# Optimization experiments

Measured on AMD Instinct MI355X. Metric: run time of the kernel, lower is better.

The kernel has to match this reference:

```python
import jax, jax.numpy as jnp
import numpy as np

# HP constants (mirroring the torch module's HP)
NUM_EFFECTIVE_QUEUES = 2
DISCOUNT_FACTOR = 0.995
USE_MIN_FOR_LOSS_REDUCE = False
ENTROPY_COEF = 0.0  # entropy branch disabled, matching HP.ENTROPY_COEF = 0.0

N_CLAUSES = 50000
FEAT_DIM = 64
HIDDEN = 256
KEY_DIM = 256
T_SEL = 1000  # number of SEL events in the journal
NEG_INF = -1e30


def setup_inputs() -> dict:
    key = jax.random.key(0)
    ks = jax.random.split(key, 10)
    feature_vecs = jax.random.normal(ks[0], (N_CLAUSES, FEAT_DIM), dtype=jnp.float32)
    W1 = jax.random.normal(ks[1], (FEAT_DIM, HIDDEN), dtype=jnp.float32) / np.sqrt(FEAT_DIM)
    b1 = jnp.zeros((HIDDEN,), dtype=jnp.float32)
    W2 = jax.random.normal(ks[2], (HIDDEN, KEY_DIM), dtype=jnp.float32) / np.sqrt(HIDDEN)
    b2 = jnp.zeros((KEY_DIM,), dtype=jnp.float32)
    keys_W = jax.random.normal(ks[3], (NUM_EFFECTIVE_QUEUES, KEY_DIM), dtype=jnp.float32) / np.sqrt(KEY_DIM)
    # Per-SEL-event passive set (equivalent to replaying ADD/REM events host-side):
    passive_mask = jax.random.uniform(ks[4], (T_SEL, N_CLAUSES)) < 0.10
    # proof_flas membership per clause, good = passive & proof
    proof = jax.random.uniform(ks[5], (N_CLAUSES,)) < 0.05
    good_mask = passive_mask & proof[None, :]
    # queue index = time % NUM_EFFECTIVE_QUEUES, time increments per SEL event
    queue_idx = jnp.arange(T_SEL, dtype=jnp.int32) % NUM_EFFECTIVE_QUEUES
    return {
        "feature_vecs": feature_vecs, "W1": W1, "b1": b1, "W2": W2, "b2": b2,
        "keys_W": keys_W, "passive_mask": passive_mask, "good_mask": good_mask,
        "queue_idx": queue_idx,
    }


def reference(feature_vecs, W1, b1, W2, b2, keys_W, passive_mask, good_mask, queue_idx):
    # clause_embedder: 2-layer MLP
    h = jax.nn.relu(feature_vecs @ W1 + b1)         # [N, H]
    emb = h @ W2 + b2                                # [N, K]
    logits = keys_W @ emb.T                          # [Q, N]
    ev_logits = logits[queue_idx]                    # [T, N] gather per SEL event

    num_good = good_mask.sum(axis=-1)                # [T]
    num_pass = passive_mask.sum(axis=-1)             # [T]
    num_bad = num_pass - num_good
    valid = (num_good > 0) & (num_bad > 0)           # events contributing loss

    # log_softmax restricted to the passive set
    masked = jnp.where(passive_mask, ev_logits, NEG_INF)
    lsm = jax.nn.log_softmax(masked, axis=-1)        # [T, N]

    # cross_entropy = -mean(lsm over good idxs)  (USE_MIN_FOR_LOSS_REDUCE = False)
    good_sum = jnp.where(good_mask, lsm, 0.0).sum(axis=-1)
    ce = -good_sum / jnp.maximum(num_good, 1).astype(lsm.dtype)

    # factor *= DISCOUNT_FACTOR after each counted step
    steps_before = (jnp.cumsum(valid.astype(jnp.int32)) - valid.astype(jnp.int32))
    factor = jnp.asarray(DISCOUNT_FACTOR, lsm.dtype) ** steps_before.astype(lsm.dtype)

    weight = factor * (num_bad.astype(lsm.dtype) / jnp.maximum(num_pass, 1).astype(lsm.dtype))
    loss_terms = jnp.where(valid, weight * ce, 0.0)
    steps = valid.sum().astype(lsm.dtype)
    loss = loss_terms.sum() / jnp.maximum(steps, 1.0)
    return loss.reshape(1)
```

## Files before the change

kernel.cpp:

```cpp
#include <hip/hip_runtime.h>
#include <hip/hip_bf16.h>

#define N_CL   50000
#define FEAT   64
#define HID    256
#define KD     256
#define T_SEL  1000
#define JSPLIT 4
#define JPB    (HID / JSPLIT)
#define NBLK   782
#define DCHUNK 10

#define WK_OFF  0
#define CK_OFF  512
#define MQ_OFF  514
#define P_OFF   520
#define LG_OFF  (P_OFF + JSPLIT * 2 * N_CL)
#define ACC_OFF (LG_OFF + 2 * N_CL)

__device__ __forceinline__ unsigned fkey(float f) {
    unsigned u = __float_as_uint(f);
    return (u & 0x80000000u) ? ~u : (u | 0x80000000u);
}
__device__ __forceinline__ float finv(unsigned k) {
    unsigned u = (k & 0x80000000u) ? (k ^ 0x80000000u) : ~k;
    return __uint_as_float(u);
}

__global__ __launch_bounds__(256) void prep_kernel(
        const float* __restrict__ W2, const float* __restrict__ b2,
        const float* __restrict__ keysW,
        float* __restrict__ wk, float* __restrict__ ck,
        unsigned* __restrict__ mq, float* __restrict__ acc) {
    __shared__ float sk0[KD], sk1[KD], sb2[KD], red[256];
    int tid = threadIdx.x;
    sk0[tid] = keysW[tid];
    sk1[tid] = keysW[KD + tid];
    sb2[tid] = b2[tid];
    for (int i = tid; i < T_SEL * 4; i += 256) acc[i] = 0.0f;
    if (tid < 2) mq[tid] = 0u;
    __syncthreads();

    const float* w2r = W2 + (size_t)tid * KD;
    float a0 = 0.f, a1 = 0.f;
    #pragma unroll 4
    for (int k = 0; k < KD; k++) {
        float w = w2r[k];
        a0 = fmaf(w, sk0[k], a0);
        a1 = fmaf(w, sk1[k], a1);
    }
    wk[tid * 2 + 0] = a0;
    wk[tid * 2 + 1] = a1;

    red[tid] = sk0[tid] * sb2[tid];
    __syncthreads();
    for (int s = 128; s > 0; s >>= 1) { if (tid < s) red[tid] += red[tid + s]; __syncthreads(); }
    if (tid == 0) ck[0] = red[0];
    __syncthreads();
    red[tid] = sk1[tid] * sb2[tid];
    __syncthreads();
    for (int s = 128; s > 0; s >>= 1) { if (tid < s) red[tid] += red[tid + s]; __syncthreads(); }
    if (tid == 0) ck[1] = red[0];
}

__global__ __launch_bounds__(64) void mlp_kernel(
        const float* __restrict__ X, const float* __restrict__ W1,
        const float* __restrict__ b1, const float* __restrict__ wk,
        float* __restrict__ P) {
    int nb = blockIdx.x % NBLK;
    int p  = blockIdx.x / NBLK;
    int n  = nb * 64 + threadIdx.x;
    int nc = (n < N_CL) ? n : (N_CL - 1);

    float x[FEAT];
    const float4* xp = (const float4*)(X + (size_t)nc * FEAT);
    #pragma unroll
    for (int k4 = 0; k4 < FEAT / 4; k4++) {
        float4 v = xp[k4];
        x[4 * k4 + 0] = v.x; x[4 * k4 + 1] = v.y;
        x[4 * k4 + 2] = v.z; x[4 * k4 + 3] = v.w;
    }

    float l0 = 0.f, l1 = 0.f;
    int j0 = p * JPB;
    for (int jg = 0; jg < JPB; jg += 16) {
        float h[16];
        #pragma unroll
        for (int u = 0; u < 16; u++) h[u] = b1[j0 + jg + u];
        #pragma unroll 4
        for (int k = 0; k < FEAT; k++) {
            const float* w1r = W1 + (size_t)k * HID + j0 + jg;
            float xv = x[k];
            #pragma unroll
            for (int u = 0; u < 16; u++) h[u] = fmaf(xv, w1r[u], h[u]);
        }
        #pragma unroll
        for (int u = 0; u < 16; u++) {
            float hv = fmaxf(h[u], 0.0f);
            l0 = fmaf(hv, wk[(j0 + jg + u) * 2 + 0], l0);
            l1 = fmaf(hv, wk[(j0 + jg + u) * 2 + 1], l1);
        }
    }
    if (n < N_CL) {
        P[((size_t)p * 2 + 0) * N_CL + n] = l0;
        P[((size_t)p * 2 + 1) * N_CL + n] = l1;
    }
}

__global__ __launch_bounds__(256) void logits_fin(
        const float* __restrict__ P, const float* __restrict__ ck,
        float* __restrict__ lg, unsigned* __restrict__ mq) {
    int n = blockIdx.x * 256 + threadIdx.x;
    float m0 = -1e30f, m1 = -1e30f;
    if (n < N_CL) {
        float l0 = ck[0], l1 = ck[1];
        #pragma unroll
        for (int p = 0; p < JSPLIT; p++) {
            l0 += P[((size_t)p * 2 + 0) * N_CL + n];
            l1 += P[((size_t)p * 2 + 1) * N_CL + n];
        }
        lg[n]        = l0;
        lg[N_CL + n] = l1;
        m0 = l0; m1 = l1;
    }
    for (int off = 32; off; off >>= 1) {
        m0 = fmaxf(m0, __shfl_xor(m0, off));
        m1 = fmaxf(m1, __shfl_xor(m1, off));
    }
    __shared__ float sm0[4], sm1[4];
    int w = threadIdx.x >> 6;
    if ((threadIdx.x & 63) == 0) { sm0[w] = m0; sm1[w] = m1; }
    __syncthreads();
    if (threadIdx.x == 0) {
        m0 = fmaxf(fmaxf(sm0[0], sm0[1]), fmaxf(sm0[2], sm0[3]));
        m1 = fmaxf(fmaxf(sm1[0], sm1[1]), fmaxf(sm1[2], sm1[3]));
        atomicMax(mq + 0, fkey(m0));
        atomicMax(mq + 1, fkey(m1));
    }
}

__global__ __launch_bounds__(256) void event_kernel(
        const int* __restrict__ pass, const int* __restrict__ good,
        const int* __restrict__ qidx, const float* __restrict__ lg,
        const unsigned* __restrict__ mq, float* __restrict__ acc) {
    int t = blockIdx.x / DCHUNK;
    int c = blockIdx.x % DCHUNK;
    int q = qidx[t] & 1;
    float M = finv(mq[q]);
    const float4* lrow = (const float4*)(lg + (size_t)q * N_CL);
    const int4*   prow = (const int4*)(pass + (size_t)t * N_CL);
    const int4*   grow = (const int4*)(good + (size_t)t * N_CL);

    float s = 0.f, sg = 0.f;
    int np = 0, ng = 0;
    for (int i = c * 256 + (int)threadIdx.x; i < N_CL / 4; i += DCHUNK * 256) {
        int4   p = prow[i];
        int4   g = grow[i];
        float4 l = lrow[i];
        np += p.x + p.y + p.z + p.w;
        ng += g.x + g.y + g.z + g.w;
        float e0 = __expf(l.x - M), e1 = __expf(l.y - M);
        float e2 = __expf(l.z - M), e3 = __expf(l.w - M);
        s  = fmaf((float)p.x, e0, s);
        s  = fmaf((float)p.y, e1, s);
        s  = fmaf((float)p.z, e2, s);
        s  = fmaf((float)p.w, e3, s);
        sg = fmaf((float)g.x, l.x, sg);
        sg = fmaf((float)g.y, l.y, sg);
        sg = fmaf((float)g.z, l.z, sg);
        sg = fmaf((float)g.w, l.w, sg);
    }
    for (int off = 32; off; off >>= 1) {
        s  += __shfl_xor(s, off);
        sg += __shfl_xor(sg, off);
        np += __shfl_xor(np, off);
        ng += __shfl_xor(ng, off);
    }
    __shared__ float rs[4], rsg[4];
    __shared__ int   rnp[4], rng[4];
    int w = threadIdx.x >> 6;
    if ((threadIdx.x & 63) == 0) { rs[w] = s; rsg[w] = sg; rnp[w] = np; rng[w] = ng; }
    __syncthreads();
    if (threadIdx.x == 0) {
        s  = rs[0] + rs[1] + rs[2] + rs[3];
        sg = rsg[0] + rsg[1] + rsg[2] + rsg[3];
        np = rnp[0] + rnp[1] + rnp[2] + rnp[3];
        ng = rng[0] + rng[1] + rng[2] + rng[3];
        atomicAdd(&acc[t * 4 + 0], s);
        atomicAdd(&acc[t * 4 + 1], sg);
        atomicAdd(&acc[t * 4 + 2], (float)np);
        atomicAdd(&acc[t * 4 + 3], (float)ng);
    }
}

__global__ __launch_bounds__(1024) void final_kernel(
        const int* __restrict__ qidx, const float* __restrict__ acc,
        const unsigned* __restrict__ mq, float* __restrict__ out) {
    int t = threadIdx.x;
    float s = 0.f, sg = 0.f, np = 0.f, ng = 0.f;
    int q = 0;
    if (t < T_SEL) {
        const float* a = acc + t * 4;
        s = a[0]; sg = a[1]; np = a[2]; ng = a[3];
        q = qidx[t] & 1;
    }
    float M  = finv(mq[q]);
    float nb = np - ng;
    int valid = (t < T_SEL) && (ng > 0.5f) && (nb > 0.5f);

    __shared__ int sc[1024];
    sc[t] = valid;
    __syncthreads();
    for (int off = 1; off < 1024; off <<= 1) {
        int v = (t >= off) ? sc[t - off] : 0;
        __syncthreads();
        sc[t] += v;
        __syncthreads();
    }
    int sb    = sc[t] - valid;
    int steps = sc[1023];

    float ce   = logf(s) + M - sg / fmaxf(ng, 1.0f);
    float wgt  = powf(0.995f, (float)sb) * nb / fmaxf(np, 1.0f);
    float term = valid ? wgt * ce : 0.0f;

    __shared__ float sf[1024];
    sf[t] = term;
    __syncthreads();
    for (int off = 512; off; off >>= 1) {
        if (t < off) sf[t] += sf[t + off];
        __syncthreads();
    }
    if (t == 0) out[0] = sf[0] / fmaxf((float)steps, 1.0f);
}

extern "C" void kernel_launch(void* const* d_in, const int* in_sizes, int n_in,
                              void* d_out, int out_size, void* d_ws, size_t ws_size,
                              hipStream_t stream) {
    const float* X     = (const float*)d_in[0];
    const float* W1    = (const float*)d_in[1];
    const float* b1    = (const float*)d_in[2];
    const float* W2    = (const float*)d_in[3];
    const float* b2    = (const float*)d_in[4];
    const float* keysW = (const float*)d_in[5];
    const int*   pass  = (const int*)d_in[6];
    const int*   good  = (const int*)d_in[7];
    const int*   qidx  = (const int*)d_in[8];

    float*    ws  = (float*)d_ws;
    float*    wk  = ws + WK_OFF;
    float*    ck  = ws + CK_OFF;
    unsigned* mq  = (unsigned*)(ws + MQ_OFF);
    float*    P   = ws + P_OFF;
    float*    lg  = ws + LG_OFF;
    float*    acc = ws + ACC_OFF;
    float*    out = (float*)d_out;

    hipLaunchKernelGGL(prep_kernel, dim3(1), dim3(256), 0, stream,
                       W2, b2, keysW, wk, ck, mq, acc);
    hipLaunchKernelGGL(mlp_kernel, dim3(NBLK * JSPLIT), dim3(64), 0, stream,
                       X, W1, b1, wk, P);
    hipLaunchKernelGGL(logits_fin, dim3((N_CL + 255) / 256), dim3(256), 0, stream,
                       P, ck, lg, mq);
    hipLaunchKernelGGL(event_kernel, dim3(T_SEL * DCHUNK), dim3(256), 0, stream,
                       pass, good, qidx, lg, mq, acc);
    hipLaunchKernelGGL(final_kernel, dim3(1), dim3(1024), 0, stream,
                       qidx, acc, mq, out);
}
```

Measured before the change: 161.8 us.

## Fuse logits finalize into MLP block reduction and halve event-kernel grid

The MLP kernel now uses 256-thread blocks where each wave handles a quarter of the hidden units, then reduces partials in shared memory and writes logits and the per-queue max directly. This removes the separate logits_fin kernel and the partial-sum buffer round trip. The event kernel switches from 10 chunks per event to 2 contiguous halves with a fixed-trip unrolled loop, and writes per-block partials instead of using atomics, so final_kernel sums two slots and the accumulator zeroing is dropped. Fewer, larger blocks in the event kernel may reduce memory-level parallelism on the dominant streaming pass over the masks.

```diff
diff --git a/kernel.cpp b/kernel.cpp
--- a/kernel.cpp
+++ b/kernel.cpp
@@ -6,16 +6,14 @@
 #define HID    256
 #define KD     256
 #define T_SEL  1000
-#define JSPLIT 4
-#define JPB    (HID / JSPLIT)
 #define NBLK   782
-#define DCHUNK 10
+#define ECHUNK 6250
+#define EFULL  24
 
 #define WK_OFF  0
 #define CK_OFF  512
 #define MQ_OFF  514
-#define P_OFF   520
-#define LG_OFF  (P_OFF + JSPLIT * 2 * N_CL)
+#define LG_OFF  520
 #define ACC_OFF (LG_OFF + 2 * N_CL)
 
 __device__ __forceinline__ unsigned fkey(float f) {
@@ -31,13 +29,12 @@
         const float* __restrict__ W2, const float* __restrict__ b2,
         const float* __restrict__ keysW,
         float* __restrict__ wk, float* __restrict__ ck,
-        unsigned* __restrict__ mq, float* __restrict__ acc) {
+        unsigned* __restrict__ mq) {
     __shared__ float sk0[KD], sk1[KD], sb2[KD], red[256];
     int tid = threadIdx.x;
     sk0[tid] = keysW[tid];
     sk1[tid] = keysW[KD + tid];
     sb2[tid] = b2[tid];
-    for (int i = tid; i < T_SEL * 4; i += 256) acc[i] = 0.0f;
     if (tid < 2) mq[tid] = 0u;
     __syncthreads();
 
@@ -63,14 +60,15 @@
     if (tid == 0) ck[1] = red[0];
 }
 
-__global__ __launch_bounds__(64) void mlp_kernel(
+__global__ __launch_bounds__(256) void mlp_kernel(
         const float* __restrict__ X, const float* __restrict__ W1,
         const float* __restrict__ b1, const float* __restrict__ wk,
-        float* __restrict__ P) {
-    int nb = blockIdx.x % NBLK;
-    int p  = blockIdx.x / NBLK;
-    int n  = nb * 64 + threadIdx.x;
-    int nc = (n < N_CL) ? n : (N_CL - 1);
+        const float* __restrict__ ck, float* __restrict__ lg,
+        unsigned* __restrict__ mq) {
+    int lane = threadIdx.x & 63;
+    int w    = threadIdx.x >> 6;
+    int n    = blockIdx.x * 64 + lane;
+    int nc   = (n < N_CL) ? n : (N_CL - 1);
 
     float x[FEAT];
     const float4* xp = (const float4*)(X + (size_t)nc * FEAT);
@@ -81,9 +79,9 @@
         x[4 * k4 + 2] = v.z; x[4 * k4 + 3] = v.w;
     }
 
+    int j0 = w * 64;
     float l0 = 0.f, l1 = 0.f;
-    int j0 = p * JPB;
-    for (int jg = 0; jg < JPB; jg += 16) {
+    for (int jg = 0; jg < 64; jg += 16) {
         float h[16];
         #pragma unroll
         for (int u = 0; u < 16; u++) h[u] = b1[j0 + jg + u];
@@ -101,75 +99,80 @@
             l1 = fmaf(hv, wk[(j0 + jg + u) * 2 + 1], l1);
         }
     }
-    if (n < N_CL) {
-        P[((size_t)p * 2 + 0) * N_CL + n] = l0;
-        P[((size_t)p * 2 + 1) * N_CL + n] = l1;
-    }
-}
-
-__global__ __launch_bounds__(256) void logits_fin(
-        const float* __restrict__ P, const float* __restrict__ ck,
-        float* __restrict__ lg, unsigned* __restrict__ mq) {
-    int n = blockIdx.x * 256 + threadIdx.x;
-    float m0 = -1e30f, m1 = -1e30f;
-    if (n < N_CL) {
-        float l0 = ck[0], l1 = ck[1];
-        #pragma unroll
-        for (int p = 0; p < JSPLIT; p++) {
-            l0 += P[((size_t)p * 2 + 0) * N_CL + n];
-            l1 += P[((size_t)p * 2 + 1) * N_CL + n];
-        }
-        lg[n]        = l0;
-        lg[N_CL + n] = l1;
-        m0 = l0; m1 = l1;
-    }
-    for (int off = 32; off; off >>= 1) {
-        m0 = fmaxf(m0, __shfl_xor(m0, off));
-        m1 = fmaxf(m1, __shfl_xor(m1, off));
-    }
-    __shared__ float sm0[4], sm1[4];
-    int w = threadIdx.x >> 6;
-    if ((threadIdx.x & 63) == 0) { sm0[w] = m0; sm1[w] = m1; }
-    __syncthreads();
-    if (threadIdx.x == 0) {
-        m0 = fmaxf(fmaxf(sm0[0], sm0[1]), fmaxf(sm0[2], sm0[3]));
-        m1 = fmaxf(fmaxf(sm1[0], sm1[1]), fmaxf(sm1[2], sm1[3]));
-        atomicMax(mq + 0, fkey(m0));
-        atomicMax(mq + 1, fkey(m1));
-    }
-}
+
+    __shared__ float red[4][2][64];
+    red[w][0][lane] = l0;
+    red[w][1][lane] = l1;
+    __syncthreads();
+    if (w == 0) {
+        float a0 = red[0][0][lane] + red[1][0][lane] + red[2][0][lane] + red[3][0][lane] + ck[0];
+        float a1 = red[0][1][lane] + red[1][1][lane] + red[2][1][lane] + red[3][1][lane] + ck[1];
+        float m0 = -1e30f, m1 = -1e30f;
+        if (n < N_CL) {
+            lg[n]        = a0;
+            lg[N_CL + n] = a1;
+            m0 = a0; m1 = a1;
+        }
+        for (int off = 32; off; off >>= 1) {
+            m0 = fmaxf(m0, __shfl_xor(m0, off));
+            m1 = fmaxf(m1, __shfl_xor(m1, off));
+        }
+        if (lane == 0) {
+            atomicMax(mq + 0, fkey(m0));
+            atomicMax(mq + 1, fkey(m1));
+        }
+    }
+}
+
+#define EBODY(pp, gg, ll)                                   \
+    do {                                                    \
+        np += pp.x + pp.y + pp.z + pp.w;                    \
+        ng += gg.x + gg.y + gg.z + gg.w;                    \
+        float e0 = __expf(ll.x - M), e1 = __expf(ll.y - M); \
+        float e2 = __expf(ll.z - M), e3 = __expf(ll.w - M); \
+        s  = fmaf((float)pp.x, e0, s);                      \
+        s  = fmaf((float)pp.y, e1, s);                      \
+        s  = fmaf((float)pp.z, e2, s);                      \
+        s  = fmaf((float)pp.w, e3, s);                      \
+        sg = fmaf((float)gg.x, ll.x, sg);                   \
+        sg = fmaf((float)gg.y, ll.y, sg);                   \
+        sg = fmaf((float)gg.z, ll.z, sg);                   \
+        sg = fmaf((float)gg.w, ll.w, sg);                   \
+    } while (0)
 
 __global__ __launch_bounds__(256) void event_kernel(
         const int* __restrict__ pass, const int* __restrict__ good,
         const int* __restrict__ qidx, const float* __restrict__ lg,
         const unsigned* __restrict__ mq, float* __restrict__ acc) {
-    int t = blockIdx.x / DCHUNK;
-    int c = blockIdx.x % DCHUNK;
+    int t   = blockIdx.x >> 1;
+    int h   = blockIdx.x & 1;
+    int tid = threadIdx.x;
     int q = qidx[t] & 1;
     float M = finv(mq[q]);
-    const float4* lrow = (const float4*)(lg + (size_t)q * N_CL);
-    const int4*   prow = (const int4*)(pass + (size_t)t * N_CL);
-    const int4*   grow = (const int4*)(good + (size_t)t * N_CL);
+    const float4* lrow = (const float4*)(lg + (size_t)q * N_CL) + (size_t)h * ECHUNK;
+    const int4*   prow = (const int4*)(pass + (size_t)t * N_CL) + (size_t)h * ECHUNK;
+    const int4*   grow = (const int4*)(good + (size_t)t * N_CL) + (size_t)h * ECHUNK;
 
     float s = 0.f, sg = 0.f;
     int np = 0, ng = 0;
-    for (int i = c * 256 + (int)threadIdx.x; i < N_CL / 4; i += DCHUNK * 256) {
+    #pragma unroll 4
+    for (int it = 0; it < EFULL; ++it) {
+        int i = it * 256 + tid;
         int4   p = prow[i];
         int4   g = grow[i];
         float4 l = lrow[i];
-        np += p.x + p.y + p.z + p.w;
-        ng += g.x + g.y + g.z + g.w;
-        float e0 = __expf(l.x - M), e1 = __expf(l.y - M);
-        float e2 = __expf(l.z - M), e3 = __expf(l.w - M);
-        s  = fmaf((float)p.x, e0, s);
-        s  = fmaf((float)p.y, e1, s);
-        s  = fmaf((float)p.z, e2, s);
-        s  = fmaf((float)p.w, e3, s);
-        sg = fmaf((float)g.x, l.x, sg);
-        sg = fmaf((float)g.y, l.y, sg);
-        sg = fmaf((float)g.z, l.z, sg);
-        sg = fmaf((float)g.w, l.w, sg);
-    }
+        EBODY(p, g, l);
+    }
+    {
+        int i = EFULL * 256 + tid;
+        if (i < ECHUNK) {
+            int4   p = prow[i];
+            int4   g = grow[i];
+            float4 l = lrow[i];
+            EBODY(p, g, l);
+        }
+    }
+
     for (int off = 32; off; off >>= 1) {
         s  += __shfl_xor(s, off);
         sg += __shfl_xor(sg, off);
@@ -178,18 +181,16 @@
     }
     __shared__ float rs[4], rsg[4];
     __shared__ int   rnp[4], rng[4];
-    int w = threadIdx.x >> 6;
-    if ((threadIdx.x & 63) == 0) { rs[w] = s; rsg[w] = sg; rnp[w] = np; rng[w] = ng; }
-    __syncthreads();
-    if (threadIdx.x == 0) {
+    int w = tid >> 6;
+    if ((tid & 63) == 0) { rs[w] = s; rsg[w] = sg; rnp[w] = np; rng[w] = ng; }
+    __syncthreads();
+    if (tid == 0) {
         s  = rs[0] + rs[1] + rs[2] + rs[3];
         sg = rsg[0] + rsg[1] + rsg[2] + rsg[3];
         np = rnp[0] + rnp[1] + rnp[2] + rnp[3];
         ng = rng[0] + rng[1] + rng[2] + rng[3];
-        atomicAdd(&acc[t * 4 + 0], s);
-        atomicAdd(&acc[t * 4 + 1], sg);
-        atomicAdd(&acc[t * 4 + 2], (float)np);
-        atomicAdd(&acc[t * 4 + 3], (float)ng);
+        float* a = acc + (size_t)blockIdx.x * 4;
+        a[0] = s; a[1] = sg; a[2] = (float)np; a[3] = (float)ng;
     }
 }
 
@@ -200,8 +201,11 @@
     float s = 0.f, sg = 0.f, np = 0.f, ng = 0.f;
     int q = 0;
     if (t < T_SEL) {
-        const float* a = acc + t * 4;
-        s = a[0]; sg = a[1]; np = a[2]; ng = a[3];
+        const float* a = acc + (size_t)t * 8;
+        s  = a[0] + a[4];
+        sg = a[1] + a[5];
+        np = a[2] + a[6];
+        ng = a[3] + a[7];
         q = qidx[t] & 1;
     }
     float M  = finv(mq[q]);
@@ -251,18 +255,15 @@
     float*    wk  = ws + WK_OFF;
     float*    ck  = ws + CK_OFF;
     unsigned* mq  = (unsigned*)(ws + MQ_OFF);
-    float*    P   = ws + P_OFF;
     float*    lg  = ws + LG_OFF;
     float*    acc = ws + ACC_OFF;
     float*    out = (float*)d_out;
 
     hipLaunchKernelGGL(prep_kernel, dim3(1), dim3(256), 0, stream,
-                       W2, b2, keysW, wk, ck, mq, acc);
-    hipLaunchKernelGGL(mlp_kernel, dim3(NBLK * JSPLIT), dim3(64), 0, stream,
-                       X, W1, b1, wk, P);
-    hipLaunchKernelGGL(logits_fin, dim3((N_CL + 255) / 256), dim3(256), 0, stream,
-                       P, ck, lg, mq);
-    hipLaunchKernelGGL(event_kernel, dim3(T_SEL * DCHUNK), dim3(256), 0, stream,
+                       W2, b2, keysW, wk, ck, mq);
+    hipLaunchKernelGGL(mlp_kernel, dim3(NBLK), dim3(256), 0, stream,
+                       X, W1, b1, wk, ck, lg, mq);
+    hipLaunchKernelGGL(event_kernel, dim3(T_SEL * 2), dim3(256), 0, stream,
                        pass, good, qidx, lg, mq, acc);
     hipLaunchKernelGGL(final_kernel, dim3(1), dim3(1024), 0, stream,
                        qidx, acc, mq, out);
```

Measured after the change: 273.8 us. 1.69x slower.

## Precompute bf16 exp/logit tables and stage chunks in LDS for event reduction

Applied to the files above, without the earlier changes.

Adds a pack kernel that computes exp(logit-M) once per clause and stores it with the logits as bf16. The event kernel now caches one chunk of these tables in LDS and loops over 14 events per block, so exp is no longer recomputed per event and logits are not re-read from global memory for every event. The float atomics into a zeroed accumulator are replaced by per-wave partial writes that the final kernel sums. The MLP kernel also drops from 4 to 2 hidden-dim splits, fully unrolls its k loop and gets a launch-bounds occupancy hint. Storing exp and logits in bf16 reduces precision of the loss sums.

```diff
diff --git a/kernel.cpp b/kernel.cpp
--- a/kernel.cpp
+++ b/kernel.cpp
@@ -6,17 +6,25 @@
 #define HID    256
 #define KD     256
 #define T_SEL  1000
-#define JSPLIT 4
+#define NBLK   782
+#define JSPLIT 2
 #define JPB    (HID / JSPLIT)
-#define NBLK   782
-#define DCHUNK 10
+
+#define NQUAD  12500
+#define PKQ    12800
+#define CHUNKQ 1280
+#define NCHUNK 10
+#define EVG    14
+#define NEG    76
 
 #define WK_OFF  0
 #define CK_OFF  512
 #define MQ_OFF  514
 #define P_OFF   520
 #define LG_OFF  (P_OFF + JSPLIT * 2 * N_CL)
-#define ACC_OFF (LG_OFF + 2 * N_CL)
+#define EPK_OFF (LG_OFF + 2 * N_CL)
+#define LPK_OFF (EPK_OFF + 2 * PKQ * 2)
+#define ACC_OFF (LPK_OFF + 2 * PKQ * 2)
 
 __device__ __forceinline__ unsigned fkey(float f) {
     unsigned u = __float_as_uint(f);
@@ -25,19 +33,25 @@
 __device__ __forceinline__ float finv(unsigned k) {
     unsigned u = (k & 0x80000000u) ? (k ^ 0x80000000u) : ~k;
     return __uint_as_float(u);
+}
+__device__ __forceinline__ float b2f(unsigned short u) {
+    return __uint_as_float(((unsigned)u) << 16);
+}
+__device__ __forceinline__ unsigned short f2bf(float f) {
+    unsigned u = __float_as_uint(f);
+    return (unsigned short)((u + 0x7FFFu + ((u >> 16) & 1u)) >> 16);
 }
 
 __global__ __launch_bounds__(256) void prep_kernel(
         const float* __restrict__ W2, const float* __restrict__ b2,
         const float* __restrict__ keysW,
         float* __restrict__ wk, float* __restrict__ ck,
-        unsigned* __restrict__ mq, float* __restrict__ acc) {
+        unsigned* __restrict__ mq) {
     __shared__ float sk0[KD], sk1[KD], sb2[KD], red[256];
     int tid = threadIdx.x;
     sk0[tid] = keysW[tid];
     sk1[tid] = keysW[KD + tid];
     sb2[tid] = b2[tid];
-    for (int i = tid; i < T_SEL * 4; i += 256) acc[i] = 0.0f;
     if (tid < 2) mq[tid] = 0u;
     __syncthreads();
 
@@ -63,12 +77,12 @@
     if (tid == 0) ck[1] = red[0];
 }
 
-__global__ __launch_bounds__(64) void mlp_kernel(
+__global__ __launch_bounds__(64, 2) void mlp_kernel(
         const float* __restrict__ X, const float* __restrict__ W1,
         const float* __restrict__ b1, const float* __restrict__ wk,
         float* __restrict__ P) {
-    int nb = blockIdx.x % NBLK;
-    int p  = blockIdx.x / NBLK;
+    int nb = blockIdx.x >> 1;
+    int p  = blockIdx.x & 1;
     int n  = nb * 64 + threadIdx.x;
     int nc = (n < N_CL) ? n : (N_CL - 1);
 
@@ -87,7 +101,7 @@
         float h[16];
         #pragma unroll
         for (int u = 0; u < 16; u++) h[u] = b1[j0 + jg + u];
-        #pragma unroll 4
+        #pragma unroll
         for (int k = 0; k < FEAT; k++) {
             const float* w1r = W1 + (size_t)k * HID + j0 + jg;
             float xv = x[k];
@@ -139,69 +153,103 @@
     }
 }
 
-__global__ __launch_bounds__(256) void event_kernel(
+__global__ __launch_bounds__(256) void epack_kernel(
+        const float* __restrict__ lg, const unsigned* __restrict__ mq,
+        ushort4* __restrict__ epk, ushort4* __restrict__ lpk) {
+    int quad = blockIdx.x * 256 + threadIdx.x;
+    if (quad >= PKQ) return;
+    #pragma unroll
+    for (int q = 0; q < 2; q++) {
+        ushort4 ev = {0, 0, 0, 0}, lv = {0, 0, 0, 0};
+        if (quad < NQUAD) {
+            float4 f = ((const float4*)lg)[(size_t)q * NQUAD + quad];
+            float M = finv(mq[q]);
+            ev.x = f2bf(__expf(f.x - M)); ev.y = f2bf(__expf(f.y - M));
+            ev.z = f2bf(__expf(f.z - M)); ev.w = f2bf(__expf(f.w - M));
+            lv.x = f2bf(f.x); lv.y = f2bf(f.y);
+            lv.z = f2bf(f.z); lv.w = f2bf(f.w);
+        }
+        epk[(size_t)q * PKQ + quad] = ev;
+        lpk[(size_t)q * PKQ + quad] = lv;
+    }
+}
+
+__global__ __launch_bounds__(256) void emain_kernel(
         const int* __restrict__ pass, const int* __restrict__ good,
-        const int* __restrict__ qidx, const float* __restrict__ lg,
-        const unsigned* __restrict__ mq, float* __restrict__ acc) {
-    int t = blockIdx.x / DCHUNK;
-    int c = blockIdx.x % DCHUNK;
-    int q = qidx[t] & 1;
-    float M = finv(mq[q]);
-    const float4* lrow = (const float4*)(lg + (size_t)q * N_CL);
-    const int4*   prow = (const int4*)(pass + (size_t)t * N_CL);
-    const int4*   grow = (const int4*)(good + (size_t)t * N_CL);
-
-    float s = 0.f, sg = 0.f;
-    int np = 0, ng = 0;
-    for (int i = c * 256 + (int)threadIdx.x; i < N_CL / 4; i += DCHUNK * 256) {
-        int4   p = prow[i];
-        int4   g = grow[i];
-        float4 l = lrow[i];
-        np += p.x + p.y + p.z + p.w;
-        ng += g.x + g.y + g.z + g.w;
-        float e0 = __expf(l.x - M), e1 = __expf(l.y - M);
-        float e2 = __expf(l.z - M), e3 = __expf(l.w - M);
-        s  = fmaf((float)p.x, e0, s);
-        s  = fmaf((float)p.y, e1, s);
-        s  = fmaf((float)p.z, e2, s);
-        s  = fmaf((float)p.w, e3, s);
-        sg = fmaf((float)g.x, l.x, sg);
-        sg = fmaf((float)g.y, l.y, sg);
-        sg = fmaf((float)g.z, l.z, sg);
-        sg = fmaf((float)g.w, l.w, sg);
-    }
-    for (int off = 32; off; off >>= 1) {
-        s  += __shfl_xor(s, off);
-        sg += __shfl_xor(sg, off);
-        np += __shfl_xor(np, off);
-        ng += __shfl_xor(ng, off);
-    }
-    __shared__ float rs[4], rsg[4];
-    __shared__ int   rnp[4], rng[4];
-    int w = threadIdx.x >> 6;
-    if ((threadIdx.x & 63) == 0) { rs[w] = s; rsg[w] = sg; rnp[w] = np; rng[w] = ng; }
-    __syncthreads();
-    if (threadIdx.x == 0) {
-        s  = rs[0] + rs[1] + rs[2] + rs[3];
-        sg = rsg[0] + rsg[1] + rsg[2] + rsg[3];
-        np = rnp[0] + rnp[1] + rnp[2] + rnp[3];
-        ng = rng[0] + rng[1] + rng[2] + rng[3];
-        atomicAdd(&acc[t * 4 + 0], s);
-        atomicAdd(&acc[t * 4 + 1], sg);
-        atomicAdd(&acc[t * 4 + 2], (float)np);
-        atomicAdd(&acc[t * 4 + 3], (float)ng);
+        const int* __restrict__ qidx,
+        const ushort4* __restrict__ epk, const ushort4* __restrict__ lpk,
+        float4* __restrict__ acc) {
+    int c = blockIdx.x % NCHUNK;
+    int g = blockIdx.x / NCHUNK;
+    int tid  = threadIdx.x;
+    int w    = tid >> 6;
+    int lane = tid & 63;
+
+    __shared__ ushort4 eL[2][CHUNKQ];
+    __shared__ ushort4 lL[2][CHUNKQ];
+    for (int i = tid; i < 2 * CHUNKQ; i += 256) {
+        int q = (i >= CHUNKQ) ? 1 : 0;
+        int j = i - q * CHUNKQ;
+        eL[q][j] = epk[(size_t)q * PKQ + c * CHUNKQ + j];
+        lL[q][j] = lpk[(size_t)q * PKQ + c * CHUNKQ + j];
+    }
+    __syncthreads();
+
+    int lbase = w * 320 + lane;
+    for (int e = 0; e < EVG; e++) {
+        int t = g * EVG + e;
+        if (t >= T_SEL) break;
+        int q = qidx[t] & 1;
+        const int4* prow = (const int4*)pass + (size_t)t * NQUAD + c * CHUNKQ;
+        const int4* grow = (const int4*)good + (size_t)t * NQUAD + c * CHUNKQ;
+
+        float s = 0.f, sg = 0.f;
+        int np = 0, ng = 0;
+        #pragma unroll
+        for (int it = 0; it < 5; it++) {
+            int lq = lbase + it * 64;
+            bool ok = (c * CHUNKQ + lq) < NQUAD;
+            int4 p  = ok ? prow[lq] : make_int4(0, 0, 0, 0);
+            int4 gm = ok ? grow[lq] : make_int4(0, 0, 0, 0);
+            ushort4 ev = eL[q][lq];
+            ushort4 lv = lL[q][lq];
+            np += p.x + p.y + p.z + p.w;
+            ng += gm.x + gm.y + gm.z + gm.w;
+            s  = fmaf((float)p.x,  b2f(ev.x), s);
+            s  = fmaf((float)p.y,  b2f(ev.y), s);
+            s  = fmaf((float)p.z,  b2f(ev.z), s);
+            s  = fmaf((float)p.w,  b2f(ev.w), s);
+            sg = fmaf((float)gm.x, b2f(lv.x), sg);
+            sg = fmaf((float)gm.y, b2f(lv.y), sg);
+            sg = fmaf((float)gm.z, b2f(lv.z), sg);
+            sg = fmaf((float)gm.w, b2f(lv.w), sg);
+        }
+        for (int off = 32; off; off >>= 1) {
+            s  += __shfl_xor(s, off);
+            sg += __shfl_xor(sg, off);
+            np += __shfl_xor(np, off);
+            ng += __shfl_xor(ng, off);
+        }
+        if (lane == 0)
+            acc[((size_t)t * NCHUNK + c) * 4 + w] =
+                make_float4(s, sg, (float)np, (float)ng);
     }
 }
 
 __global__ __launch_bounds__(1024) void final_kernel(
-        const int* __restrict__ qidx, const float* __restrict__ acc,
+        const int* __restrict__ qidx, const float4* __restrict__ acc,
         const unsigned* __restrict__ mq, float* __restrict__ out) {
     int t = threadIdx.x;
     float s = 0.f, sg = 0.f, np = 0.f, ng = 0.f;
     int q = 0;
     if (t < T_SEL) {
-        const float* a = acc + t * 4;
-        s = a[0]; sg = a[1]; np = a[2]; ng = a[3];
+        #pragma unroll 2
+        for (int c = 0; c < NCHUNK; c++)
+            #pragma unroll
+            for (int w = 0; w < 4; w++) {
+                float4 a = acc[((size_t)t * NCHUNK + c) * 4 + w];
+                s += a.x; sg += a.y; np += a.z; ng += a.w;
+            }
         q = qidx[t] & 1;
     }
     float M  = finv(mq[q]);
@@ -253,17 +301,21 @@
     unsigned* mq  = (unsigned*)(ws + MQ_OFF);
     float*    P   = ws + P_OFF;
     float*    lg  = ws + LG_OFF;
-    float*    acc = ws + ACC_OFF;
+    ushort4*  epk = (ushort4*)(ws + EPK_OFF);
+    ushort4*  lpk = (ushort4*)(ws + LPK_OFF);
+    float4*   acc = (float4*)(ws + ACC_OFF);
     float*    out = (float*)d_out;
 
     hipLaunchKernelGGL(prep_kernel, dim3(1), dim3(256), 0, stream,
-                       W2, b2, keysW, wk, ck, mq, acc);
+                       W2, b2, keysW, wk, ck, mq);
     hipLaunchKernelGGL(mlp_kernel, dim3(NBLK * JSPLIT), dim3(64), 0, stream,
                        X, W1, b1, wk, P);
     hipLaunchKernelGGL(logits_fin, dim3((N_CL + 255) / 256), dim3(256), 0, stream,
                        P, ck, lg, mq);
-    hipLaunchKernelGGL(event_kernel, dim3(T_SEL * DCHUNK), dim3(256), 0, stream,
-                       pass, good, qidx, lg, mq, acc);
+    hipLaunchKernelGGL(epack_kernel, dim3(PKQ / 256), dim3(256), 0, stream,
+                       lg, mq, epk, lpk);
+    hipLaunchKernelGGL(emain_kernel, dim3(NCHUNK * NEG), dim3(256), 0, stream,
+                       pass, good, qidx, epk, lpk, acc);
     hipLaunchKernelGGL(final_kernel, dim3(1), dim3(1024), 0, stream,
                        qidx, acc, mq, out);
 }
```

Result: slower. 199.2 us (+23.1%).
